# Performance work log

Measured on AMD Instinct MI355X. Metric: run time of the kernel, lower is better.

Reference implementation:

```python
import jax, jax.numpy as jnp
import numpy as np

NUM_HEADS = 16
PAD_ID = 0.0  # max(config.pad_id, 0)


def setup_inputs() -> dict:
    key = jax.random.key(0)
    ks = jax.random.split(key, 9)
    B, T, C = 2, 2048, 1024
    x = jax.random.normal(ks[0], (B, T, C), dtype=jnp.float32)
    # xavier_uniform-like scale for square [C, C] weights
    lim = (6.0 / (C + C)) ** 0.5
    def w(k):
        return jax.random.uniform(k, (C, C), dtype=jnp.float32, minval=-lim, maxval=lim)
    def b(k):
        return jax.random.uniform(k, (C,), dtype=jnp.float32)  # nn.init.uniform_ default [0,1)
    return {
        "x": x,
        "wq_w": w(ks[1]), "wq_b": b(ks[2]),
        "wk_w": w(ks[3]), "wk_b": b(ks[4]),
        "wv_w": w(ks[5]), "wv_b": b(ks[6]),
        "wo_w": w(ks[7]), "wo_b": b(ks[8]),
    }


def reference(x, wq_w, wq_b, wk_w, wk_b, wv_w, wv_b, wo_w, wo_b):
    B, T, C = x.shape
    H = NUM_HEADS
    Dh = C // H
    scale = Dh ** -0.5

    # Linear layers (torch Linear: x @ W.T + b), then split heads -> [B, T, H, Dh]
    q = (x @ wq_w.T + wq_b).reshape(B, T, H, Dh)
    k = (x @ wk_w.T + wk_b).reshape(B, T, H, Dh)
    v = (x @ wv_w.T + wv_b).reshape(B, T, H, Dh)

    # scores: [B, H, Tq, Tk]
    scores = jnp.einsum("bthd,bshd->bhts", q, k) * scale

    # Padding mask over keys: (x[:,:,0] != pad_id) -> [B, 1, 1, Tk]
    key_mask = (x[:, :, 0] != PAD_ID)[:, None, None, :]
    scores = jnp.where(key_mask, scores, -jnp.inf)

    attn = jax.nn.softmax(scores, axis=-1)

    out = jnp.einsum("bhts,bshd->bthd", attn, v).reshape(B, T, C)
    return out @ wo_w.T + wo_b
```

## Files before the change

### kernel.cpp

```cpp
#include <hip/hip_runtime.h>
#include <hip/hip_bf16.h>

typedef short short8 __attribute__((ext_vector_type(8)));
typedef float f32x4 __attribute__((ext_vector_type(4)));

#define MFMA32(a, b, c) __builtin_amdgcn_mfma_f32_16x16x32_bf16(a, b, c, 0, 0, 0)

#if __has_builtin(__builtin_amdgcn_exp2f)
#define EXP2F(x) __builtin_amdgcn_exp2f(x)
#else
#define EXP2F(x) exp2f(x)
#endif

#define GLL16(gp, lp) __builtin_amdgcn_global_load_lds(                                  \
    (__attribute__((address_space(1))) unsigned int*)(unsigned long long)(const void*)(gp), \
    (__attribute__((address_space(3))) unsigned int*)(lp), 16, 0, 0)

__device__ __forceinline__ unsigned short f2b(float f) {
    union { float f; unsigned int u; } v;
    v.f = f;
    unsigned int u = v.u;
    return (unsigned short)((u + 0x7fffu + ((u >> 16) & 1u)) >> 16);
}

static __device__ __forceinline__ f32x4 max4(f32x4 x, f32x4 y) {
    f32x4 r;
    r[0] = fmaxf(x[0], y[0]); r[1] = fmaxf(x[1], y[1]);
    r[2] = fmaxf(x[2], y[2]); r[3] = fmaxf(x[3], y[3]);
    return r;
}

__global__ void cvt_all(const float* __restrict__ x,
                        const float* __restrict__ w0, const float* __restrict__ w1,
                        const float* __restrict__ w2, const float* __restrict__ w3,
                        unsigned short* __restrict__ xb, unsigned short* __restrict__ wb,
                        float* __restrict__ maskbuf) {
    int blk = blockIdx.x;
    if (blk < 4096) {
        int i = blk * 256 + threadIdx.x;
        float4 v = ((const float4*)x)[i];
        ushort4 o;
        o.x = f2b(v.x); o.y = f2b(v.y); o.z = f2b(v.z); o.w = f2b(v.w);
        ((ushort4*)xb)[i] = o;
        if ((i & 255) == 0)
            maskbuf[i >> 8] = (v.x != 0.0f) ? 0.0f : -1e30f;
    } else {
        int wi = blk - 4096;
        int widx = wi >> 10;
        int i = (wi & 1023) * 256 + threadIdx.x;
        const float* src = widx == 0 ? w0 : (widx == 1 ? w1 : (widx == 2 ? w2 : w3));
        float4 v = ((const float4*)src)[i];
        ushort4 o;
        o.x = f2b(v.x); o.y = f2b(v.y); o.z = f2b(v.z); o.w = f2b(v.w);
        ((ushort4*)(wb + ((size_t)widx << 20)))[i] = o;
    }
}

#define QSCALE (0.125f * 1.44269504088896341f)

__global__ __launch_bounds__(256) void gemm_qkv(
        const unsigned short* __restrict__ A,
        const unsigned short* __restrict__ wq, const unsigned short* __restrict__ wk,
        const unsigned short* __restrict__ wv,
        const float* __restrict__ bq, const float* __restrict__ bk,
        const float* __restrict__ bv,
        unsigned short* __restrict__ qbuf, unsigned short* __restrict__ kbuf,
        unsigned short* __restrict__ vbuf) {
    __shared__ __attribute__((aligned(16))) unsigned short As[2][128 * 32];
    __shared__ __attribute__((aligned(16))) unsigned short Bs[2][128 * 32];
    int tid = threadIdx.x;
    int lane = tid & 63, wave = tid >> 6;
    int lane15 = lane & 15, quad = lane >> 4;
    int seg = blockIdx.x >> 3;
    int bn = (blockIdx.x & 7) * 128;
    int bm = blockIdx.y * 128;
    const unsigned short* Bw = seg == 0 ? wq : (seg == 1 ? wk : wv);
    const float* bias = seg == 0 ? bq : (seg == 1 ? bk : bv);
    int wm = (wave >> 1) * 64, wn = (wave & 1) * 64;

    f32x4 acc[4][4];
#pragma unroll
    for (int i = 0; i < 4; i++)
#pragma unroll
        for (int j = 0; j < 4; j++) acc[i][j] = (f32x4){0.f, 0.f, 0.f, 0.f};

    int arow = tid >> 2, acol = (tid & 3) * 8;
    const unsigned short* A0 = &A[(size_t)(bm + arow) * 1024 + acol];
    const unsigned short* A1 = A0 + (size_t)64 * 1024;
    const unsigned short* B0 = &Bw[(size_t)(bn + arow) * 1024 + acol];
    const unsigned short* B1 = B0 + (size_t)64 * 1024;

    GLL16(A0, &As[0][(size_t)tid * 8]);
    GLL16(A1, &As[0][(size_t)(tid + 256) * 8]);
    GLL16(B0, &Bs[0][(size_t)tid * 8]);
    GLL16(B1, &Bs[0][(size_t)(tid + 256) * 8]);

    for (int it = 0; it < 32; it++) {
        int cur = it & 1;
        __syncthreads();
        if (it < 31) {
            int kn = (it + 1) * 32;
            GLL16(A0 + kn, &As[cur ^ 1][(size_t)tid * 8]);
            GLL16(A1 + kn, &As[cur ^ 1][(size_t)(tid + 256) * 8]);
            GLL16(B0 + kn, &Bs[cur ^ 1][(size_t)tid * 8]);
            GLL16(B1 + kn, &Bs[cur ^ 1][(size_t)(tid + 256) * 8]);
        }
        const unsigned short* as = As[cur];
        const unsigned short* bs = Bs[cur];
        short8 af[4], bf[4];
#pragma unroll
        for (int i = 0; i < 4; i++)
            af[i] = *(const short8*)&as[(wm + i * 16 + lane15) * 32 + quad * 8];
#pragma unroll
        for (int j = 0; j < 4; j++)
            bf[j] = *(const short8*)&bs[(wn + j * 16 + lane15) * 32 + quad * 8];
#pragma unroll
        for (int i = 0; i < 4; i++)
#pragma unroll
            for (int j = 0; j < 4; j++)
                acc[i][j] = MFMA32(af[i], bf[j], acc[i][j]);
    }

    int bb = bm >> 11;
#pragma unroll
    for (int j = 0; j < 4; j++) {
        int nl = bn + wn + j * 16 + lane15;
        int h = nl >> 6, d = nl & 63;
        float bv_ = bias[nl];
        if (seg == 2) {
            size_t vbase = ((size_t)((bb * 16 + h) * 64 + d)) * 2048;
#pragma unroll
            for (int i = 0; i < 4; i++) {
                int tk0 = (bm & 2047) + wm + i * 16 + quad * 4;
                int grp = tk0 >> 5;
                ushort4 pk;
                pk.x = f2b(acc[i][j][0] + bv_);
                pk.y = f2b(acc[i][j][1] + bv_);
                pk.z = f2b(acc[i][j][2] + bv_);
                pk.w = f2b(acc[i][j][3] + bv_);
                *(ushort4*)&vbuf[vbase + grp * 32 + quad * 8 + (i & 1) * 4] = pk;
            }
        } else {
#pragma unroll
            for (int i = 0; i < 4; i++)
#pragma unroll
                for (int r = 0; r < 4; r++) {
                    int m = bm + wm + i * 16 + quad * 4 + r;
                    int tk = m & 2047;
                    float v = acc[i][j][r] + bv_;
                    size_t off = ((size_t)((bb * 16 + h) * 2048 + tk)) * 64 + d;
                    if (seg == 0) qbuf[off] = f2b(v * QSCALE);
                    else          kbuf[off] = f2b(v);
                }
        }
    }
}

__global__ __launch_bounds__(256) void gemm_proj(
        const unsigned short* __restrict__ A, const unsigned short* __restrict__ Bw,
        const float* __restrict__ bias, float* __restrict__ out) {
    __shared__ __attribute__((aligned(16))) unsigned short As[2][64 * 32];
    __shared__ __attribute__((aligned(16))) unsigned short Bs[2][128 * 32];
    int tid = threadIdx.x;
    int lane = tid & 63, wave = tid >> 6;
    int lane15 = lane & 15, quad = lane >> 4;
    int bn = blockIdx.x * 128, bm = blockIdx.y * 64;
    int wm = (wave >> 1) * 32, wn = (wave & 1) * 64;

    f32x4 acc[2][4];
#pragma unroll
    for (int i = 0; i < 2; i++)
#pragma unroll
        for (int j = 0; j < 4; j++) acc[i][j] = (f32x4){0.f, 0.f, 0.f, 0.f};

    int arow = tid >> 2, acol = (tid & 3) * 8;
    const unsigned short* A0 = &A[(size_t)(bm + arow) * 1024 + acol];
    const unsigned short* B0 = &Bw[(size_t)(bn + arow) * 1024 + acol];
    const unsigned short* B1 = B0 + (size_t)64 * 1024;

    GLL16(A0, &As[0][(size_t)tid * 8]);
    GLL16(B0, &Bs[0][(size_t)tid * 8]);
    GLL16(B1, &Bs[0][(size_t)(tid + 256) * 8]);

    for (int it = 0; it < 32; it++) {
        int cur = it & 1;
        __syncthreads();
        if (it < 31) {
            int kn = (it + 1) * 32;
            GLL16(A0 + kn, &As[cur ^ 1][(size_t)tid * 8]);
            GLL16(B0 + kn, &Bs[cur ^ 1][(size_t)tid * 8]);
            GLL16(B1 + kn, &Bs[cur ^ 1][(size_t)(tid + 256) * 8]);
        }
        const unsigned short* as = As[cur];
        const unsigned short* bs = Bs[cur];
        short8 af[2], bf[4];
#pragma unroll
        for (int i = 0; i < 2; i++)
            af[i] = *(const short8*)&as[(wm + i * 16 + lane15) * 32 + quad * 8];
#pragma unroll
        for (int j = 0; j < 4; j++)
            bf[j] = *(const short8*)&bs[(wn + j * 16 + lane15) * 32 + quad * 8];
#pragma unroll
        for (int i = 0; i < 2; i++)
#pragma unroll
            for (int j = 0; j < 4; j++)
                acc[i][j] = MFMA32(af[i], bf[j], acc[i][j]);
    }

#pragma unroll
    for (int j = 0; j < 4; j++) {
        int n = bn + wn + j * 16 + lane15;
        float bv_ = bias[n];
#pragma unroll
        for (int i = 0; i < 2; i++)
#pragma unroll
            for (int r = 0; r < 4; r++) {
                int m = bm + wm + i * 16 + quad * 4 + r;
                out[(size_t)m * 1024 + n] = acc[i][j][r] + bv_;
            }
    }
}

__global__ __launch_bounds__(256, 2) void attn_kernel(
        const unsigned short* __restrict__ qbuf, const unsigned short* __restrict__ kbuf,
        const unsigned short* __restrict__ vtbuf, const float* __restrict__ maskbuf,
        unsigned short* __restrict__ attnout) {
    __shared__ __attribute__((aligned(16))) unsigned short Ks[2][128 * 64];
    __shared__ __attribute__((aligned(16))) unsigned short Vs[2][64 * 128];

    int id = blockIdx.x;
    int combo = (id & 7) | (((id >> 7) & 3) << 3);
    int qt = (id >> 3) & 15;
    int b = combo >> 4, h = combo & 15;
    int tid = threadIdx.x, lane = tid & 63, wave = tid >> 6;
    int lane15 = lane & 15, quad = lane >> 4;
    int q0 = qt * 128 + wave * 32;

    const unsigned short* Q  = qbuf  + (size_t)combo * 2048 * 64;
    const unsigned short* Kp = kbuf  + (size_t)combo * 2048 * 64;
    const unsigned short* Vt = vtbuf + (size_t)combo * 64 * 2048;
    const float* mb = maskbuf + b * 2048;

    short8 qf[2][2];
#pragma unroll
    for (int a = 0; a < 2; a++)
#pragma unroll
        for (int g = 0; g < 2; g++)
            qf[a][g] = *(const short8*)&Q[(size_t)(q0 + a * 16 + lane15) * 64 + g * 32 + quad * 8];

    int ci0 = tid;
    float m_run[2] = {-1e30f, -1e30f}, l_run[2] = {0.f, 0.f};
    f32x4 o[2][4];
#pragma unroll
    for (int a = 0; a < 2; a++)
#pragma unroll
        for (int c = 0; c < 4; c++) o[a][c] = (f32x4){0.f, 0.f, 0.f, 0.f};

    const f32x4 z4 = {0.f, 0.f, 0.f, 0.f};
    int x7 = lane15 & 7;

#pragma unroll
    for (int r4 = 0; r4 < 4; r4++) {
        int ci = ci0 + r4 * 256;
        int kr = ci >> 3, kc = (ci & 7) ^ (kr & 7);
        GLL16(&Kp[(size_t)kr * 64 + kc * 8], &Ks[0][(size_t)ci * 8]);
        int vd = ci >> 4, vc = (ci & 15) ^ (vd & 15);
        GLL16(&Vt[(size_t)vd * 2048 + vc * 8], &Vs[0][(size_t)ci * 8]);
    }

    for (int it = 0; it < 16; it++) {
        int cur = it & 1;
        int kb = it * 128;
        __syncthreads();
        if (it < 15) {
            int kn = kb + 128;
#pragma unroll
            for (int r4 = 0; r4 < 4; r4++) {
                int ci = ci0 + r4 * 256;
                int kr = ci >> 3, kc = (ci & 7) ^ (kr & 7);
                GLL16(&Kp[(size_t)(kn + kr) * 64 + kc * 8], &Ks[cur ^ 1][(size_t)ci * 8]);
                int vd = ci >> 4, vc = (ci & 15) ^ (vd & 15);
                GLL16(&Vt[(size_t)vd * 2048 + kn + vc * 8], &Vs[cur ^ 1][(size_t)ci * 8]);
            }
        }
        const unsigned short* ks = Ks[cur];
        const unsigned short* vs = Vs[cur];

        f32x4 s[2][8];
#pragma unroll
        for (int t = 0; t < 8; t++) {
            int row = t * 16 + lane15;
            short8 k0 = *(const short8*)&ks[row * 64 + (quad ^ x7) * 8];
            short8 k1 = *(const short8*)&ks[row * 64 + ((quad + 4) ^ x7) * 8];
            f32x4 t0 = MFMA32(k0, qf[0][0], z4);
            s[0][t] = MFMA32(k1, qf[0][1], t0);
            f32x4 t1 = MFMA32(k0, qf[1][0], z4);
            s[1][t] = MFMA32(k1, qf[1][1], t1);
        }
#pragma unroll
        for (int t = 0; t < 8; t++) {
            f32x4 mkt = *(const f32x4*)&mb[kb + t * 16 + quad * 4];
            s[0][t] += mkt;
            s[1][t] += mkt;
        }
        short8 pb8[2][4];
#pragma unroll
        for (int a = 0; a < 2; a++) {
            f32x4 m4 = s[a][0];
#pragma unroll
            for (int t = 1; t < 8; t++) m4 = max4(m4, s[a][t]);
            float mx = fmaxf(fmaxf(m4[0], m4[1]), fmaxf(m4[2], m4[3]));
            mx = fmaxf(mx, __shfl_xor(mx, 16));
            mx = fmaxf(mx, __shfl_xor(mx, 32));
            float mnew = fmaxf(m_run[a], mx);
            float alpha = EXP2F(m_run[a] - mnew);
            m_run[a] = mnew;
            float ls = 0.f;
#pragma unroll
            for (int g = 0; g < 4; g++) {
                float e0 = EXP2F(s[a][2 * g][0] - mnew);
                float e1 = EXP2F(s[a][2 * g][1] - mnew);
                float e2 = EXP2F(s[a][2 * g][2] - mnew);
                float e3 = EXP2F(s[a][2 * g][3] - mnew);
                float f0 = EXP2F(s[a][2 * g + 1][0] - mnew);
                float f1 = EXP2F(s[a][2 * g + 1][1] - mnew);
                float f2 = EXP2F(s[a][2 * g + 1][2] - mnew);
                float f3 = EXP2F(s[a][2 * g + 1][3] - mnew);
                ls += ((e0 + e1) + (e2 + e3)) + ((f0 + f1) + (f2 + f3));
                union { uint4 u; short8 sv; } pu;
                pu.u.x = __builtin_amdgcn_perm(__float_as_uint(e1), __float_as_uint(e0), 0x07060302u);
                pu.u.y = __builtin_amdgcn_perm(__float_as_uint(e3), __float_as_uint(e2), 0x07060302u);
                pu.u.z = __builtin_amdgcn_perm(__float_as_uint(f1), __float_as_uint(f0), 0x07060302u);
                pu.u.w = __builtin_amdgcn_perm(__float_as_uint(f3), __float_as_uint(f2), 0x07060302u);
                pb8[a][g] = pu.sv;
            }
            l_run[a] = l_run[a] * alpha + ls;
#pragma unroll
            for (int c = 0; c < 4; c++) o[a][c] *= alpha;
        }
#pragma unroll
        for (int c = 0; c < 4; c++) {
            int d = c * 16 + lane15;
#pragma unroll
            for (int g = 0; g < 4; g++) {
                int skc = (g * 4 + quad) ^ lane15;
                short8 vv = *(const short8*)&vs[d * 128 + skc * 8];
                o[0][c] = MFMA32(vv, pb8[0][g], o[0][c]);
                o[1][c] = MFMA32(vv, pb8[1][g], o[1][c]);
            }
        }
    }

#pragma unroll
    for (int a = 0; a < 2; a++) {
        float l = l_run[a];
        l += __shfl_xor(l, 16);
        l += __shfl_xor(l, 32);
        float rl = 1.0f / l;
        size_t row = (size_t)(b * 2048 + q0 + a * 16 + lane15) * 1024 + h * 64 + quad * 4;
#pragma unroll
        for (int c = 0; c < 4; c++) {
            ushort4 pk;
            pk.x = f2b(o[a][c][0] * rl);
            pk.y = f2b(o[a][c][1] * rl);
            pk.z = f2b(o[a][c][2] * rl);
            pk.w = f2b(o[a][c][3] * rl);
            *(ushort4*)&attnout[row + c * 16] = pk;
        }
    }
}

extern "C" void kernel_launch(void* const* d_in, const int* in_sizes, int n_in,
                              void* d_out, int out_size, void* d_ws, size_t ws_size,
                              hipStream_t stream) {
    const float* x    = (const float*)d_in[0];
    const float* wq_w = (const float*)d_in[1];
    const float* wq_b = (const float*)d_in[2];
    const float* wk_w = (const float*)d_in[3];
    const float* wk_b = (const float*)d_in[4];
    const float* wv_w = (const float*)d_in[5];
    const float* wv_b = (const float*)d_in[6];
    const float* wo_w = (const float*)d_in[7];
    const float* wo_b = (const float*)d_in[8];
    float* out = (float*)d_out;

    char* ws = (char*)d_ws;
    size_t off = 0;
    unsigned short* xb      = (unsigned short*)(ws + off); off += (size_t)4096 * 1024 * 2;
    unsigned short* wb      = (unsigned short*)(ws + off); off += (size_t)4 * 1024 * 1024 * 2;
    unsigned short* qbuf    = (unsigned short*)(ws + off); off += (size_t)4096 * 1024 * 2;
    unsigned short* kbuf    = (unsigned short*)(ws + off); off += (size_t)4096 * 1024 * 2;
    unsigned short* vbuf    = (unsigned short*)(ws + off); off += (size_t)4096 * 1024 * 2;
    unsigned short* attnout = (unsigned short*)(ws + off); off += (size_t)4096 * 1024 * 2;
    float* maskbuf          = (float*)(ws + off);          off += 4096 * 4;

    unsigned short* wqb = wb;
    unsigned short* wkb = wb + (1u << 20);
    unsigned short* wvb = wb + (2u << 20);
    unsigned short* wob = wb + (3u << 20);

    cvt_all<<<8192, 256, 0, stream>>>(x, wq_w, wk_w, wv_w, wo_w, xb, wb, maskbuf);

    gemm_qkv<<<dim3(24, 32), 256, 0, stream>>>(xb, wqb, wkb, wvb,
                                               wq_b, wk_b, wv_b, qbuf, kbuf, vbuf);

    attn_kernel<<<512, 256, 0, stream>>>(qbuf, kbuf, vbuf, maskbuf, attnout);

    gemm_proj<<<dim3(8, 64), 256, 0, stream>>>(attnout, wob, wo_b, out);
}
```

Measured before the change: 218.8 us.

## Pre-tile V into MFMA fragment layout and load directly from global

```diff
diff --git a/kernel.cpp b/kernel.cpp
--- a/kernel.cpp
+++ b/kernel.cpp
@@ -95,6 +95,9 @@
     GLL16(B0, &Bs[0][(size_t)tid * 8]);
     GLL16(B1, &Bs[0][(size_t)(tid + 256) * 8]);
 
+    int rb = (seg == 2) ? wm : wn;
+    int cb = (seg == 2) ? wn : wm;
+
     for (int it = 0; it < 32; it++) {
         int cur = it & 1;
         __syncthreads();
@@ -105,53 +108,66 @@
             GLL16(B0 + kn, &Bs[cur ^ 1][(size_t)tid * 8]);
             GLL16(B1 + kn, &Bs[cur ^ 1][(size_t)(tid + 256) * 8]);
         }
-        const unsigned short* as = As[cur];
-        const unsigned short* bs = Bs[cur];
-        short8 af[4], bf[4];
+        const unsigned short* rs = (seg == 2) ? As[cur] : Bs[cur];
+        const unsigned short* cs = (seg == 2) ? Bs[cur] : As[cur];
+        short8 rf[4], cf[4];
 #pragma unroll
         for (int i = 0; i < 4; i++)
-            af[i] = *(const short8*)&as[(wm + i * 16 + lane15) * 32 + quad * 8];
+            rf[i] = *(const short8*)&rs[(rb + i * 16 + lane15) * 32 + quad * 8];
 #pragma unroll
         for (int j = 0; j < 4; j++)
-            bf[j] = *(const short8*)&bs[(wn + j * 16 + lane15) * 32 + quad * 8];
+            cf[j] = *(const short8*)&cs[(cb + j * 16 + lane15) * 32 + quad * 8];
 #pragma unroll
         for (int i = 0; i < 4; i++)
 #pragma unroll
             for (int j = 0; j < 4; j++)
-                acc[i][j] = MFMA32(af[i], bf[j], acc[i][j]);
+                acc[i][j] = MFMA32(rf[i], cf[j], acc[i][j]);
     }
 
     int bb = bm >> 11;
-#pragma unroll
-    for (int j = 0; j < 4; j++) {
-        int nl = bn + wn + j * 16 + lane15;
-        int h = nl >> 6, d = nl & 63;
-        float bv_ = bias[nl];
-        if (seg == 2) {
-            size_t vbase = ((size_t)((bb * 16 + h) * 64 + d)) * 2048;
+    if (seg == 2) {
+#pragma unroll
+        for (int j = 0; j < 4; j++) {
+            int nl = bn + wn + j * 16 + lane15;
+            int h = nl >> 6, d = nl & 63;
+            float bv_ = bias[nl];
+            size_t vbase = (size_t)(bb * 16 + h) * 131072;
 #pragma unroll
             for (int i = 0; i < 4; i++) {
                 int tk0 = (bm & 2047) + wm + i * 16 + quad * 4;
-                int grp = tk0 >> 5;
+                int B7 = tk0 >> 7, g2 = (tk0 >> 5) & 3;
                 ushort4 pk;
                 pk.x = f2b(acc[i][j][0] + bv_);
                 pk.y = f2b(acc[i][j][1] + bv_);
                 pk.z = f2b(acc[i][j][2] + bv_);
                 pk.w = f2b(acc[i][j][3] + bv_);
-                *(ushort4*)&vbuf[vbase + grp * 32 + quad * 8 + (i & 1) * 4] = pk;
+                size_t off = vbase + (size_t)(((B7 * 16 + g2 * 4 + quad) * 64 + d)) * 8
+                             + (i & 1) * 4;
+                *(ushort4*)&vbuf[off] = pk;
             }
-        } else {
-#pragma unroll
-            for (int i = 0; i < 4; i++)
-#pragma unroll
-                for (int r = 0; r < 4; r++) {
-                    int m = bm + wm + i * 16 + quad * 4 + r;
-                    int tk = m & 2047;
-                    float v = acc[i][j][r] + bv_;
-                    size_t off = ((size_t)((bb * 16 + h) * 2048 + tk)) * 64 + d;
-                    if (seg == 0) qbuf[off] = f2b(v * QSCALE);
-                    else          kbuf[off] = f2b(v);
+        }
+    } else {
+#pragma unroll
+        for (int i = 0; i < 4; i++) {
+            int n0 = bn + wn + i * 16 + quad * 4;
+            int h = n0 >> 6, d0 = n0 & 63;
+            f32x4 bv4 = *(const f32x4*)&bias[n0];
+            unsigned short* dst = (seg == 0) ? qbuf : kbuf;
+#pragma unroll
+            for (int j = 0; j < 4; j++) {
+                int m = bm + wm + j * 16 + lane15;
+                int tk = m & 2047;
+                f32x4 v = acc[i][j] + bv4;
+                ushort4 pk;
+                if (seg == 0) {
+                    pk.x = f2b(v[0] * QSCALE); pk.y = f2b(v[1] * QSCALE);
+                    pk.z = f2b(v[2] * QSCALE); pk.w = f2b(v[3] * QSCALE);
+                } else {
+                    pk.x = f2b(v[0]); pk.y = f2b(v[1]);
+                    pk.z = f2b(v[2]); pk.w = f2b(v[3]);
                 }
+                *(ushort4*)&dst[((size_t)((bb * 16 + h) * 2048 + tk)) * 64 + d0] = pk;
+            }
         }
     }
 }
@@ -167,11 +183,11 @@
     int bn = blockIdx.x * 128, bm = blockIdx.y * 64;
     int wm = (wave >> 1) * 32, wn = (wave & 1) * 64;
 
-    f32x4 acc[2][4];
-#pragma unroll
-    for (int i = 0; i < 2; i++)
-#pragma unroll
-        for (int j = 0; j < 4; j++) acc[i][j] = (f32x4){0.f, 0.f, 0.f, 0.f};
+    f32x4 acc[4][2];
+#pragma unroll
+    for (int i = 0; i < 4; i++)
+#pragma unroll
+        for (int j = 0; j < 2; j++) acc[i][j] = (f32x4){0.f, 0.f, 0.f, 0.f};
 
     int arow = tid >> 2, acol = (tid & 3) * 8;
     const unsigned short* A0 = &A[(size_t)(bm + arow) * 1024 + acol];
@@ -195,29 +211,28 @@
         const unsigned short* bs = Bs[cur];
         short8 af[2], bf[4];
 #pragma unroll
-        for (int i = 0; i < 2; i++)
-            af[i] = *(const short8*)&as[(wm + i * 16 + lane15) * 32 + quad * 8];
-#pragma unroll
-        for (int j = 0; j < 4; j++)
-            bf[j] = *(const short8*)&bs[(wn + j * 16 + lane15) * 32 + quad * 8];
-#pragma unroll
-        for (int i = 0; i < 2; i++)
-#pragma unroll
-            for (int j = 0; j < 4; j++)
-                acc[i][j] = MFMA32(af[i], bf[j], acc[i][j]);
-    }
-
-#pragma unroll
-    for (int j = 0; j < 4; j++) {
-        int n = bn + wn + j * 16 + lane15;
-        float bv_ = bias[n];
-#pragma unroll
-        for (int i = 0; i < 2; i++)
-#pragma unroll
-            for (int r = 0; r < 4; r++) {
-                int m = bm + wm + i * 16 + quad * 4 + r;
-                out[(size_t)m * 1024 + n] = acc[i][j][r] + bv_;
-            }
+        for (int j = 0; j < 2; j++)
+            af[j] = *(const short8*)&as[(wm + j * 16 + lane15) * 32 + quad * 8];
+#pragma unroll
+        for (int i = 0; i < 4; i++)
+            bf[i] = *(const short8*)&bs[(wn + i * 16 + lane15) * 32 + quad * 8];
+#pragma unroll
+        for (int i = 0; i < 4; i++)
+#pragma unroll
+            for (int j = 0; j < 2; j++)
+                acc[i][j] = MFMA32(bf[i], af[j], acc[i][j]);
+    }
+
+#pragma unroll
+    for (int i = 0; i < 4; i++) {
+        int n0 = bn + wn + i * 16 + quad * 4;
+        f32x4 bv4 = *(const f32x4*)&bias[n0];
+#pragma unroll
+        for (int j = 0; j < 2; j++) {
+            int m = bm + wm + j * 16 + lane15;
+            f32x4 v = acc[i][j] + bv4;
+            *(f32x4*)&out[(size_t)m * 1024 + n0] = v;
+        }
     }
 }
 
@@ -226,7 +241,6 @@
         const unsigned short* __restrict__ vtbuf, const float* __restrict__ maskbuf,
         unsigned short* __restrict__ attnout) {
     __shared__ __attribute__((aligned(16))) unsigned short Ks[2][128 * 64];
-    __shared__ __attribute__((aligned(16))) unsigned short Vs[2][64 * 128];
 
     int id = blockIdx.x;
     int combo = (id & 7) | (((id >> 7) & 3) << 3);
@@ -238,7 +252,7 @@
 
     const unsigned short* Q  = qbuf  + (size_t)combo * 2048 * 64;
     const unsigned short* Kp = kbuf  + (size_t)combo * 2048 * 64;
-    const unsigned short* Vt = vtbuf + (size_t)combo * 64 * 2048;
+    const unsigned short* Vt = vtbuf + (size_t)combo * 131072;
     const float* mb = maskbuf + b * 2048;
 
     short8 qf[2][2];
@@ -248,7 +262,6 @@
         for (int g = 0; g < 2; g++)
             qf[a][g] = *(const short8*)&Q[(size_t)(q0 + a * 16 + lane15) * 64 + g * 32 + quad * 8];
 
-    int ci0 = tid;
     float m_run[2] = {-1e30f, -1e30f}, l_run[2] = {0.f, 0.f};
     f32x4 o[2][4];
 #pragma unroll
@@ -261,11 +274,9 @@
 
 #pragma unroll
     for (int r4 = 0; r4 < 4; r4++) {
-        int ci = ci0 + r4 * 256;
+        int ci = tid + r4 * 256;
         int kr = ci >> 3, kc = (ci & 7) ^ (kr & 7);
         GLL16(&Kp[(size_t)kr * 64 + kc * 8], &Ks[0][(size_t)ci * 8]);
-        int vd = ci >> 4, vc = (ci & 15) ^ (vd & 15);
-        GLL16(&Vt[(size_t)vd * 2048 + vc * 8], &Vs[0][(size_t)ci * 8]);
     }
 
     for (int it = 0; it < 16; it++) {
@@ -273,18 +284,14 @@
         int kb = it * 128;
         __syncthreads();
         if (it < 15) {
-            int kn = kb + 128;
 #pragma unroll
             for (int r4 = 0; r4 < 4; r4++) {
-                int ci = ci0 + r4 * 256;
+                int ci = tid + r4 * 256;
                 int kr = ci >> 3, kc = (ci & 7) ^ (kr & 7);
-                GLL16(&Kp[(size_t)(kn + kr) * 64 + kc * 8], &Ks[cur ^ 1][(size_t)ci * 8]);
-                int vd = ci >> 4, vc = (ci & 15) ^ (vd & 15);
-                GLL16(&Vt[(size_t)vd * 2048 + kn + vc * 8], &Vs[cur ^ 1][(size_t)ci * 8]);
+                GLL16(&Kp[(size_t)(kb + 128 + kr) * 64 + kc * 8], &Ks[cur ^ 1][(size_t)ci * 8]);
             }
         }
         const unsigned short* ks = Ks[cur];
-        const unsigned short* vs = Vs[cur];
 
         f32x4 s[2][8];
 #pragma unroll
@@ -297,6 +304,15 @@
             f32x4 t1 = MFMA32(k0, qf[1][0], z4);
             s[1][t] = MFMA32(k1, qf[1][1], t1);
         }
+
+        short8 vv[16];
+#pragma unroll
+        for (int c = 0; c < 4; c++)
+#pragma unroll
+            for (int g = 0; g < 4; g++)
+                vv[c * 4 + g] = *(const short8*)&Vt[
+                    (size_t)(((it * 16 + g * 4 + quad) * 64) + c * 16 + lane15) * 8];
+
 #pragma unroll
         for (int t = 0; t < 8; t++) {
             f32x4 mkt = *(const f32x4*)&mb[kb + t * 16 + quad * 4];
@@ -339,16 +355,12 @@
             for (int c = 0; c < 4; c++) o[a][c] *= alpha;
         }
 #pragma unroll
-        for (int c = 0; c < 4; c++) {
-            int d = c * 16 + lane15;
+        for (int c = 0; c < 4; c++)
 #pragma unroll
             for (int g = 0; g < 4; g++) {
-                int skc = (g * 4 + quad) ^ lane15;
-                short8 vv = *(const short8*)&vs[d * 128 + skc * 8];
-                o[0][c] = MFMA32(vv, pb8[0][g], o[0][c]);
-                o[1][c] = MFMA32(vv, pb8[1][g], o[1][c]);
+                o[0][c] = MFMA32(vv[c * 4 + g], pb8[0][g], o[0][c]);
+                o[1][c] = MFMA32(vv[c * 4 + g], pb8[1][g], o[1][c]);
             }
-        }
     }
 
 #pragma unroll
```

New measurement: 232.2 us. 1.06x slower.
